# Performance work log

Hardware: AMD Instinct MI355X
Metric: run time of the kernel (lower is better)

## Reference

```python
import jax, jax.numpy as jnp
import numpy as np
from jax import lax

B, IN_N, OUT_N, SEQ, HID = 8, 16, 16, 256, 64
NUM_C = 64 + 3  # grid_size + spline_order
EPS_LN = 1e-5


def setup_inputs():
    key = jax.random.key(0)
    k = jax.random.split(key, 8)
    f32 = jnp.float32
    return {
        "x_in": jax.random.normal(k[0], (B, IN_N, SEQ, HID), f32),
        "proj_x_prev": jax.random.normal(k[1], (B, IN_N, SEQ, HID), f32),
        "spline_weights": jax.random.normal(k[2], (IN_N, OUT_N, NUM_C), f32) * 0.1,
        "base_scales": 0.6 + 0.1 * jax.random.normal(k[3], (IN_N, OUT_N), f32),
        "tau": jax.random.normal(k[4], (IN_N, OUT_N), f32) * 0.1 + 0.1,
        "temperature": jnp.array(1.0, f32),
        "omiga": jnp.full((IN_N, OUT_N), 0.2, f32),
        "W2": jax.random.normal(k[5], (OUT_N, HID, HID), f32) / np.sqrt(HID).astype(np.float32),
        "b_param": jnp.zeros((OUT_N, SEQ, HID), f32),
        "ln_w": jnp.ones((OUT_N, HID), f32),
        "ln_b": jnp.zeros((OUT_N, HID), f32),
        "alpha": jnp.full((OUT_N,), 0.5, f32),
        "beta": jnp.ones((OUT_N,), f32),
        "gamma": jnp.full((OUT_N,), 0.5, f32),
        "theta": jnp.ones((OUT_N,), f32),
        "conv_w": jax.random.normal(k[6], (OUT_N, HID, 1, 3, 3), f32) * 0.1,
    }


def _layernorm(x, w=None, b=None):
    mu = jnp.mean(x, -1, keepdims=True)
    var = jnp.mean((x - mu) ** 2, -1, keepdims=True)
    y = (x - mu) / jnp.sqrt(var + EPS_LN)
    if w is not None:
        y = y * w + b
    return y


def _dwconv(x, w):
    # x: [b, C, 16, 16]; w: [C, 1, 3, 3]; depthwise conv, SAME padding
    return lax.conv_general_dilated(
        x, w, (1, 1), "SAME",
        dimension_numbers=("NCHW", "OIHW", "NCHW"),
        feature_group_count=x.shape[1])


def _forward(x_in, proj_x_prev, spline_weights, base_scales, tau, temperature,
             omiga, W2, b_param, ln_w, ln_b, alpha, beta, gamma, theta, conv_w):
    b, in_n, seq, feat = x_in.shape
    num_c = spline_weights.shape[-1]
    grid = jnp.linspace(-1.0, 1.0, num_c)
    h = 2.0 / (num_c - 1)

    x_energy = jnp.mean(x_in, -1)  # [b,i,s]
    x_norm = jnp.clip(
        x_energy / (jnp.max(jnp.abs(x_energy), -1, keepdims=True) + 1e-8),
        -0.99, 0.99)

    # cubic B-spline basis (masked branches -> nested where)
    dist = jnp.abs(x_norm[..., None] - grid) / h  # [b,i,s,c]
    basis = jnp.where(dist < 1.0, 2.0 / 3.0 - dist ** 2 + dist ** 3 / 2.0,
            jnp.where(dist < 2.0, (2.0 - dist) ** 3 / 6.0, jnp.zeros_like(dist)))

    base_feat = jax.nn.silu(x_norm)[:, :, None, :] * base_scales[None, :, :, None]  # [b,i,j,s]
    spline_feat = jnp.einsum("bisc,ijc->bijs", basis, spline_weights)
    edge_resp = base_feat + spline_feat
    # [b,i,j,s,f]
    activated = (edge_resp[..., None] + jnp.abs(omiga)[None, :, :, None, None]) * x_in[:, :, None]

    t_val = jnp.abs(temperature) + 1e-4
    edge_energies = jnp.mean(jnp.abs(activated), axis=(-1, -2))  # [b,i,j]
    tau_abs = jnp.abs(tau)  # [i,j]
    mask = jax.nn.sigmoid((edge_energies - tau_abs[None]) / t_val)  # [b,i,j]

    # attention kernel W1, vectorized over output neuron j
    mid = in_n // 2
    mult = edge_energies / (tau_abs[None] + 1e-8)  # [b,i,j]
    wp = proj_x_prev[:, :, None] * (mult * mask)[..., None, None]  # [b,i,j,s,d]
    d = wp.shape[-1]
    K = jnp.transpose(wp[:, :mid], (0, 2, 3, 1, 4)).reshape(b, -1, seq, mid * d)
    Q = jnp.transpose(wp[:, mid:2 * mid], (0, 2, 3, 1, 4)).reshape(b, -1, seq, mid * d)
    K, Q = _layernorm(K), _layernorm(Q)
    raw = jnp.einsum("bjsk,bjtk->bjst", K, Q) / (jnp.sqrt(jnp.float32(mid * d)) * t_val)
    W1 = jax.nn.softmax(raw, axis=-1)  # [b,j,s,s]

    # masked mean over input neurons -> per-neuron SplineWeightLayer (vectorized)
    x = jnp.mean(activated * mask[..., None, None], axis=1)  # [b,j,s,f]
    xn = _layernorm(x, ln_w[None, :, None, :], ln_b[None, :, None, :])
    x_prime = jnp.einsum("bjsf,jfo->bjso", xn, W2) + b_param[None]  # [b,j,s,o]
    o = x_prime.shape[-1]

    # depthwise 3x3 conv on 16x16 spatial view, per-j kernels
    xsp = jnp.transpose(x_prime, (1, 0, 3, 2)).reshape(-1, b, o, 16, 16)  # [j,b,o,16,16]
    w3 = jax.vmap(_dwconv)(xsp, conv_w)  # [j,b,o,16,16]
    w3 = jnp.transpose(w3.reshape(-1, b, o, seq), (1, 0, 3, 2))  # [b,j,s,o]

    eye = jnp.eye(seq, dtype=x_prime.dtype)
    ak = (jnp.abs(beta)[None, :, None, None] * W1
          + jnp.abs(alpha)[None, :, None, None] * eye[None, None])
    glob = jnp.einsum("bjst,bjto->bjso", ak, x_prime)
    combined = glob + jnp.abs(theta)[None, :, None, None] * w3
    # residual_proj is Identity since in_hidden == out_hidden
    out = combined + gamma[None, :, None, None] * x
    return out, x_prime  # both [b, out_n, seq, out_hidden]


def reference(x_in, proj_x_prev, spline_weights, base_scales, tau, temperature,
              omiga, W2, b_param, ln_w, ln_b, alpha, beta, gamma, theta, conv_w):
    return _forward(x_in, proj_x_prev, spline_weights, base_scales, tau, temperature,
                    omiga, W2, b_param, ln_w, ln_b, alpha, beta, gamma, theta, conv_w)
```

## Files before the change

kernel.cpp:

```cpp
#include <hip/hip_runtime.h>

#define EPSLN 1e-5f

typedef short bf16x8 __attribute__((ext_vector_type(8)));
typedef float f32x4 __attribute__((ext_vector_type(4)));
typedef unsigned short u16;
typedef unsigned short u16x8 __attribute__((ext_vector_type(8)));

__device__ __forceinline__ float wsum(float v){
  #pragma unroll
  for(int o=32;o;o>>=1) v += __shfl_xor(v,o);
  return v;
}
__device__ __forceinline__ float wmax(float v){
  #pragma unroll
  for(int o=32;o;o>>=1) v = fmaxf(v,__shfl_xor(v,o));
  return v;
}
__device__ __forceinline__ u16 f2bf(float f){
  unsigned int u = __float_as_uint(f);
  u = (u + 0x7FFFu + ((u>>16)&1u)) >> 16;
  return (u16)u;
}
__device__ __forceinline__ float bf2f(u16 h){
  return __uint_as_float(((unsigned int)h)<<16);
}

__global__ void __launch_bounds__(256) kA(
                   const float* __restrict__ xin, const float* __restrict__ p,
                   const float* __restrict__ W2,
                   float* __restrict__ xe, float* __restrict__ xa,
                   float* __restrict__ Sv, float* __restrict__ SSv,
                   u16* __restrict__ xinb, u16* __restrict__ phi, u16* __restrict__ plo,
                   u16* __restrict__ w2B){
  int t = threadIdx.x;
  int rl = t>>3, q = t&7;
  int row = blockIdx.x*32 + rl;
  const float4* xr = (const float4*)(xin + row*64 + q*8);
  const float4* pr = (const float4*)(p   + row*64 + q*8);
  float s1=0.f,s2=0.f,s3=0.f,s4=0.f;
  u16x8 xb, ph, pl;
  #pragma unroll
  for(int k=0;k<2;k++){
    float4 xv = xr[k];
    float4 pv = pr[k];
    s1 += xv.x+xv.y+xv.z+xv.w;
    s2 += fabsf(xv.x)+fabsf(xv.y)+fabsf(xv.z)+fabsf(xv.w);
    s3 += pv.x+pv.y+pv.z+pv.w;
    s4 += pv.x*pv.x+pv.y*pv.y+pv.z*pv.z+pv.w*pv.w;
    int o = k*4;
    xb[o+0]=f2bf(xv.x); xb[o+1]=f2bf(xv.y); xb[o+2]=f2bf(xv.z); xb[o+3]=f2bf(xv.w);
    u16 h0=f2bf(pv.x), h1=f2bf(pv.y), h2=f2bf(pv.z), h3=f2bf(pv.w);
    ph[o+0]=h0; ph[o+1]=h1; ph[o+2]=h2; ph[o+3]=h3;
    pl[o+0]=f2bf(pv.x-bf2f(h0)); pl[o+1]=f2bf(pv.y-bf2f(h1));
    pl[o+2]=f2bf(pv.z-bf2f(h2)); pl[o+3]=f2bf(pv.w-bf2f(h3));
  }
  *(u16x8*)(xinb + row*64 + q*8) = xb;
  *(u16x8*)(phi  + row*64 + q*8) = ph;
  *(u16x8*)(plo  + row*64 + q*8) = pl;
  s1 += __shfl_xor(s1,1); s1 += __shfl_xor(s1,2); s1 += __shfl_xor(s1,4);
  s2 += __shfl_xor(s2,1); s2 += __shfl_xor(s2,2); s2 += __shfl_xor(s2,4);
  s3 += __shfl_xor(s3,1); s3 += __shfl_xor(s3,2); s3 += __shfl_xor(s3,4);
  s4 += __shfl_xor(s4,1); s4 += __shfl_xor(s4,2); s4 += __shfl_xor(s4,4);
  if(q==0){ xe[row]=s1*(1.f/64.f); xa[row]=s2*(1.f/64.f); Sv[row]=s3; SSv[row]=s4; }
  if(blockIdx.x<16){
    int j = blockIdx.x;
    for(int idx=threadIdx.x; idx<4096; idx+=256){
      int f = idx>>6, o = idx&63;
      float v = W2[j*4096 + idx];
      int ks = f>>5, kb = (f>>3)&3, i = f&7;
      int nt = o>>4, col = o&15;
      int ln = kb*16 + col;
      w2B[((j*2+ks)*4 + nt)*512 + ln*8 + i] = f2bf(v);
    }
  }
}

__global__ void __launch_bounds__(256) kBE(
                   const float* __restrict__ xe, const float* __restrict__ sw,
                   const float* __restrict__ bs, const float* __restrict__ om,
                   const float* __restrict__ xa, const float* __restrict__ tau,
                   const float* __restrict__ temp,
                   u16* __restrict__ er2b, float* __restrict__ mask,
                   float* __restrict__ cc,
                   const u16* __restrict__ phi, const u16* __restrict__ plo,
                   float* __restrict__ G){
  __shared__ __align__(16) unsigned char shm[32768];
  int tid = threadIdx.x;
  if(blockIdx.x < 128){
    float* swL = (float*)shm;
    float* bsL = swL + 1072;
    float* omL = bsL + 16;
    float* red = omL + 16;
    float* redE= red + 4;
    int bi = blockIdx.x;
    int i = bi & 15;
    int w = tid>>6, lane = tid&63;
    for(int k=tid;k<16*67;k+=256) swL[k] = sw[i*16*67 + k];
    if(tid<16){ bsL[tid]=bs[i*16+tid]; omL[tid]=fabsf(om[i*16+tid]); }
    float v = xe[bi*256+tid];
    float m = wmax(fabsf(v));
    if(lane==0) red[w]=m;
    __syncthreads();
    m = fmaxf(fmaxf(red[0],red[1]),fmaxf(red[2],red[3]));
    float xn = v/(m+1e-8f);
    xn = fminf(fmaxf(xn,-0.99f),0.99f);
    float sil = xn/(1.f+expf(-xn));
    float vv = (xn+1.f)*33.f;
    int c0 = (int)floorf(vv)-1;
    float acc[16];
    #pragma unroll
    for(int j=0;j<16;j++) acc[j]=0.f;
    #pragma unroll
    for(int k=0;k<4;k++){
      int c = c0+k;
      if(c<0||c>66) continue;
      float d = fabsf(vv-(float)c);
      float bas = d<1.f ? (2.f/3.f - d*d + d*d*d*0.5f)
                : (d<2.f ? (2.f-d)*(2.f-d)*(2.f-d)*(1.f/6.f) : 0.f);
      #pragma unroll
      for(int j=0;j<16;j++) acc[j] += bas*swL[j*67+c];
    }
    float xav = xa[bi*256+tid];
    u16 evb[16];
    #pragma unroll
    for(int j=0;j<16;j++){
      float ev = sil*bsL[j] + acc[j] + omL[j];
      evb[j] = f2bf(ev);
      float pe = wsum(fabsf(ev)*xav);
      if(lane==0) redE[j*4+w]=pe;
    }
    *(u16x8*)(er2b + ((size_t)bi*256+tid)*16    ) = *(u16x8*)&evb[0];
    *(u16x8*)(er2b + ((size_t)bi*256+tid)*16 + 8) = *(u16x8*)&evb[8];
    __syncthreads();
    if(tid<16){
      float e = (redE[tid*4+0]+redE[tid*4+1]+redE[tid*4+2]+redE[tid*4+3])*(1.f/256.f);
      float tv = fabsf(temp[0])+1e-4f;
      float ta = fabsf(tau[i*16+tid]);
      float mk = 1.f/(1.f+expf(-(e-ta)/tv));
      mask[bi*16+tid]=mk;
      cc[bi*16+tid]= e/(ta+1e-8f)*mk;
    }
  } else {
    u16* AfB = (u16*)shm;
    u16* BfB = AfB + 8192;
    int e = blockIdx.x - 128;
    int b = e&7, m = (e>>3)&7, sx = (e>>6)&3, ty = e>>8;
    int bm = b*8+m;
    int s0 = sx*64, t0 = ty*64;
    int row = tid>>2, dseg = tid&3;
    size_t offA = ((size_t)(b*16+m  )*256 + s0 + row)*64 + dseg*16;
    size_t offB = ((size_t)(b*16+m+8)*256 + t0 + row)*64 + dseg*16;
    int d0 = dseg*16;
    int ks0 = d0>>5, kb0 = (d0>>3)&3;
    int ks1 = (d0+8)>>5, kb1 = ((d0+8)>>3)&3;
    int lr = row&15, stile = row>>4;
    #define AOFF(h,stl,ks,ln) (((((h)*4+(stl))*2+(ks))*64 + (ln))*8)
    {
      uint4 v0 = *(const uint4*)(phi + offA);
      uint4 v1 = *(const uint4*)(phi + offA + 8);
      *(uint4*)(AfB + AOFF(0,stile,ks0,kb0*16+lr)) = v0;
      *(uint4*)(AfB + AOFF(0,stile,ks1,kb1*16+lr)) = v1;
      uint4 w0 = *(const uint4*)(plo + offA);
      uint4 w1 = *(const uint4*)(plo + offA + 8);
      *(uint4*)(AfB + AOFF(1,stile,ks0,kb0*16+lr)) = w0;
      *(uint4*)(AfB + AOFF(1,stile,ks1,kb1*16+lr)) = w1;
      uint4 x0 = *(const uint4*)(phi + offB);
      uint4 x1 = *(const uint4*)(phi + offB + 8);
      *(uint4*)(BfB + AOFF(0,stile,ks0,kb0*16+lr)) = x0;
      *(uint4*)(BfB + AOFF(0,stile,ks1,kb1*16+lr)) = x1;
      uint4 y0 = *(const uint4*)(plo + offB);
      uint4 y1 = *(const uint4*)(plo + offB + 8);
      *(uint4*)(BfB + AOFF(1,stile,ks0,kb0*16+lr)) = y0;
      *(uint4*)(BfB + AOFF(1,stile,ks1,kb1*16+lr)) = y1;
    }
    __syncthreads();
    int w = tid>>6, lane = tid&63;
    bf16x8 ah0 = *(const bf16x8*)(AfB + AOFF(0,w,0,lane));
    bf16x8 ah1 = *(const bf16x8*)(AfB + AOFF(0,w,1,lane));
    bf16x8 al0 = *(const bf16x8*)(AfB + AOFF(1,w,0,lane));
    bf16x8 al1 = *(const bf16x8*)(AfB + AOFF(1,w,1,lane));
    f32x4 acc[4];
    #pragma unroll
    for(int tt=0;tt<4;tt++) acc[tt] = (f32x4){0.f,0.f,0.f,0.f};
    #pragma unroll
    for(int tt=0;tt<4;tt++){
      bf16x8 bh0 = *(const bf16x8*)(BfB + AOFF(0,tt,0,lane));
      bf16x8 bh1 = *(const bf16x8*)(BfB + AOFF(0,tt,1,lane));
      bf16x8 bl0 = *(const bf16x8*)(BfB + AOFF(1,tt,0,lane));
      bf16x8 bl1 = *(const bf16x8*)(BfB + AOFF(1,tt,1,lane));
      acc[tt] = __builtin_amdgcn_mfma_f32_16x16x32_bf16(ah0, bh0, acc[tt], 0,0,0);
      acc[tt] = __builtin_amdgcn_mfma_f32_16x16x32_bf16(ah1, bh1, acc[tt], 0,0,0);
      acc[tt] = __builtin_amdgcn_mfma_f32_16x16x32_bf16(ah0, bl0, acc[tt], 0,0,0);
      acc[tt] = __builtin_amdgcn_mfma_f32_16x16x32_bf16(ah1, bl1, acc[tt], 0,0,0);
      acc[tt] = __builtin_amdgcn_mfma_f32_16x16x32_bf16(al0, bh0, acc[tt], 0,0,0);
      acc[tt] = __builtin_amdgcn_mfma_f32_16x16x32_bf16(al1, bh1, acc[tt], 0,0,0);
    }
    int col = lane&15, r4 = lane>>4;
    #pragma unroll
    for(int tt=0;tt<4;tt++){
      #pragma unroll
      for(int r=0;r<4;r++){
        G[((size_t)bm*256 + s0 + w*16 + r4*4 + r)*256 + t0 + tt*16 + col] = acc[tt][r];
      }
    }
    #undef AOFF
  }
}

__global__ void __launch_bounds__(256) kD(
                   const u16* __restrict__ xinb, const u16* __restrict__ er2b,
                   const float* __restrict__ mask, const u16* __restrict__ w2B,
                   const float* __restrict__ lnw, const float* __restrict__ lnb,
                   const float* __restrict__ bp,
                   u16* __restrict__ xoutb, float* __restrict__ xp,
                   u16* __restrict__ xpB,
                   const float* __restrict__ Sv, const float* __restrict__ SSv,
                   const float* __restrict__ cc,
                   float* __restrict__ mKv, float* __restrict__ rKv,
                   float* __restrict__ mQv, float* __restrict__ rQv){
  int bid = blockIdx.x;
  int tid = threadIdx.x;
  if(bid >= 1024){
    int sid = bid - 1024;
    int b = sid&7, j = sid>>3;
    int t = tid;
    float sk=0,ssk=0,sq=0,ssq=0;
    #pragma unroll
    for(int m=0;m<8;m++){
      float ck = cc[(b*16+m)*16+j];
      float cq = cc[(b*16+m+8)*16+j];
      sk  += ck*Sv[(b*16+m)*256+t];
      ssk += ck*ck*SSv[(b*16+m)*256+t];
      sq  += cq*Sv[(b*16+m+8)*256+t];
      ssq += cq*cq*SSv[(b*16+m+8)*256+t];
    }
    float mk = sk*(1.f/512.f);
    float vk = ssk*(1.f/512.f) - mk*mk;
    float mq = sq*(1.f/512.f);
    float vq = ssq*(1.f/512.f) - mq*mq;
    int o = (b*16+j)*256+t;
    mKv[o]=mk; rKv[o]=rsqrtf(vk+EPSLN);
    mQv[o]=mq; rQv[o]=rsqrtf(vq+EPSLN);
    return;
  }
  int b = bid&7, jq = (bid>>3)&7, st = bid>>6;
  int j0 = jq*2;
  int w = tid>>6, lane = tid&63;
  __shared__ __align__(16) u16 xnS[2][16*64];
  __shared__ float mcL[32];
  if(tid<32) mcL[tid] = mask[(b*16+(tid>>1))*16 + j0 + (tid&1)];
  __syncthreads();
  int ss = lane>>4, fq = lane&15;
  int sl = w*4 + ss;
  int s  = st*16 + sl;
  float a00=0.f,a01=0.f,a02=0.f,a03=0.f;
  float a10=0.f,a11=0.f,a12=0.f,a13=0.f;
  #pragma unroll
  for(int i=0;i<16;i++){
    unsigned int epk = *(const unsigned int*)(er2b + ((size_t)((b*16+i)*256+s))*16 + j0);
    float e0 = bf2f((u16)(epk&0xFFFFu))*mcL[i*2+0];
    float e1 = bf2f((u16)(epk>>16))   *mcL[i*2+1];
    ushort4 xv = *(const ushort4*)(xinb + ((size_t)(b*16+i)*256+s)*64 + fq*4);
    float x0=bf2f(xv.x), x1=bf2f(xv.y), x2=bf2f(xv.z), x3=bf2f(xv.w);
    a00 += e0*x0; a01 += e0*x1; a02 += e0*x2; a03 += e0*x3;
    a10 += e1*x0; a11 += e1*x1; a12 += e1*x2; a13 += e1*x3;
  }
  #pragma unroll
  for(int jj=0;jj<2;jj++){
    int j = j0+jj;
    int bj = b*16+j;
    float acc0 = (jj? a10:a00)*(1.f/16.f);
    float acc1 = (jj? a11:a01)*(1.f/16.f);
    float acc2 = (jj? a12:a02)*(1.f/16.f);
    float acc3 = (jj? a13:a03)*(1.f/16.f);
    {
      u16 pk[4]={f2bf(acc0),f2bf(acc1),f2bf(acc2),f2bf(acc3)};
      *(ushort4*)(xoutb + ((size_t)bj*256+s)*64 + fq*4) = *(ushort4*)pk;
    }
    float part = acc0+acc1+acc2+acc3;
    part += __shfl_xor(part,1); part += __shfl_xor(part,2);
    part += __shfl_xor(part,4); part += __shfl_xor(part,8);
    float mu = part*(1.f/64.f);
    float d0=acc0-mu, d1=acc1-mu, d2=acc2-mu, d3=acc3-mu;
    float p2 = d0*d0+d1*d1+d2*d2+d3*d3;
    p2 += __shfl_xor(p2,1); p2 += __shfl_xor(p2,2);
    p2 += __shfl_xor(p2,4); p2 += __shfl_xor(p2,8);
    float rstd = rsqrtf(p2*(1.f/64.f)+EPSLN);
    float4 lw4 = *(const float4*)(lnw + j*64 + fq*4);
    float4 lb4 = *(const float4*)(lnb + j*64 + fq*4);
    u16 xn[4] = { f2bf(d0*rstd*lw4.x + lb4.x), f2bf(d1*rstd*lw4.y + lb4.y),
                  f2bf(d2*rstd*lw4.z + lb4.z), f2bf(d3*rstd*lw4.w + lb4.w) };
    *(ushort4*)((unsigned char*)&xnS[jj][0] + ((sl*128 + fq*8) ^ ((sl&7)<<4))) = *(ushort4*)xn;
  }
  __syncthreads();
  int m = lane&15, kb = lane>>4;
  #pragma unroll
  for(int jj=0;jj<2;jj++){
    int j = j0+jj;
    int bj = b*16+j;
    f32x4 acc = {0.f,0.f,0.f,0.f};
    unsigned char* xnB = (unsigned char*)&xnS[jj][0];
    #pragma unroll
    for(int ks=0;ks<2;ks++){
      bf16x8 a = *(const bf16x8*)(xnB + ((m*128 + ks*64 + kb*16) ^ ((m&7)<<4)));
      bf16x8 bfr = *(const bf16x8*)(w2B + ((j*2+ks)*4 + w)*512 + lane*8);
      acc = __builtin_amdgcn_mfma_f32_16x16x32_bf16(a, bfr, acc, 0, 0, 0);
    }
    int f = w*16 + m;
    u16 pk[4];
    #pragma unroll
    for(int r=0;r<4;r++){
      int si = kb*4 + r;
      int s2 = st*16 + si;
      float xpr = acc[r] + bp[((size_t)j*256+s2)*64+f];
      xp[((size_t)bj*256+s2)*64+f] = xpr;
      pk[r] = f2bf(xpr);
    }
    int s0 = st*16 + kb*4;
    int flat = ((s0>>5)*4 + w)*512 + ((s0>>3)&3)*128 + m*8 + (s0&7);
    *(ushort4*)(xpB + (size_t)bj*16384 + flat) = *(ushort4*)pk;
  }
}

__global__ void __launch_bounds__(256) kF(
    const float* __restrict__ G, const float* __restrict__ cc,
    const float* __restrict__ mKv, const float* __restrict__ rKv,
    const float* __restrict__ mQv, const float* __restrict__ rQv,
    const float* __restrict__ xp, const u16* __restrict__ xpB,
    const float* __restrict__ cw,
    const u16* __restrict__ xarrb, const float* __restrict__ temp,
    const float* __restrict__ alpha, const float* __restrict__ beta,
    const float* __restrict__ gamma_, const float* __restrict__ theta,
    float* __restrict__ out){
  int b = blockIdx.x, jp = blockIdx.y, st = blockIdx.z;
  int j0 = jp*4;
  int tid = threadIdx.x, w = tid>>6, lane = tid&63;
  __shared__ __align__(16) unsigned char ovl[26112];
  unsigned char* prA = ovl;
  unsigned char* prB = ovl + 8192;
  float* xpT = (float*)ovl;
  float tv = fabsf(temp[0])+1e-4f;
  float inv = 1.f/(sqrtf(512.f)*tv);
  float aM0[8],aM1[8],aM2[8],aM3[8];
  #pragma unroll
  for(int m=0;m<8;m++){
    float4 ck = *(const float4*)(cc + (b*16+m  )*16 + j0);
    float4 cq = *(const float4*)(cc + (b*16+m+8)*16 + j0);
    aM0[m]=ck.x*cq.x; aM1[m]=ck.y*cq.y; aM2[m]=ck.z*cq.z; aM3[m]=ck.w*cq.w;
  }
  int bj0 = b*16+j0;
  float4 mQ4a = *(const float4*)(mQv + (size_t)(bj0  )*256 + lane*4);
  float4 rQ4a = *(const float4*)(rQv + (size_t)(bj0  )*256 + lane*4);
  float4 mQ4b = *(const float4*)(mQv + (size_t)(bj0+1)*256 + lane*4);
  float4 rQ4b = *(const float4*)(rQv + (size_t)(bj0+1)*256 + lane*4);
  float4 mQ4c = *(const float4*)(mQv + (size_t)(bj0+2)*256 + lane*4);
  float4 rQ4c = *(const float4*)(rQv + (size_t)(bj0+2)*256 + lane*4);
  float4 mQ4d = *(const float4*)(mQv + (size_t)(bj0+3)*256 + lane*4);
  float4 rQ4d = *(const float4*)(rQv + (size_t)(bj0+3)*256 + lane*4);
  const float* Gb = G + (size_t)(b*8)*65536;
  ushort4 pk2[4], pk3[4];
  #pragma unroll
  for(int q=0;q<4;q++){
    int si = w*4+q;
    int s = st*16 + si;
    f32x4 dt0={0.f,0.f,0.f,0.f}, dt1={0.f,0.f,0.f,0.f};
    f32x4 dt2={0.f,0.f,0.f,0.f}, dt3={0.f,0.f,0.f,0.f};
    #pragma unroll
    for(int m=0;m<8;m++){
      f32x4 g4 = *(const f32x4*)(Gb + (size_t)m*65536 + s*256 + lane*4);
      dt0 += aM0[m]*g4; dt1 += aM1[m]*g4;
      dt2 += aM2[m]*g4; dt3 += aM3[m]*g4;
    }
    #define SMK(JJ, DT, MQ, RQ, PKOUT) { \
      float mKs = 512.f*mKv[(size_t)(bj0+JJ)*256 + s], rKs = rKv[(size_t)(bj0+JJ)*256 + s]; \
      float e0 = __expf((DT[0] - mKs*MQ.x)*rKs*RQ.x*inv); \
      float e1 = __expf((DT[1] - mKs*MQ.y)*rKs*RQ.y*inv); \
      float e2 = __expf((DT[2] - mKs*MQ.z)*rKs*RQ.z*inv); \
      float e3 = __expf((DT[3] - mKs*MQ.w)*rKs*RQ.w*inv); \
      float isf = 1.f/wsum(e0+e1+e2+e3); \
      u16 pk[4] = {f2bf(e0*isf), f2bf(e1*isf), f2bf(e2*isf), f2bf(e3*isf)}; \
      PKOUT = *(ushort4*)pk; }
    ushort4 t0v, t1v;
    SMK(0, dt0, mQ4a, rQ4a, t0v)
    SMK(1, dt1, mQ4b, rQ4b, t1v)
    int poff = (si*512 + lane*8) ^ ((si&7)<<4);
    *(ushort4*)(prA + poff) = t0v;
    *(ushort4*)(prB + poff) = t1v;
    SMK(2, dt2, mQ4c, rQ4c, pk2[q])
    SMK(3, dt3, mQ4d, rQ4d, pk3[q])
    #undef SMK
  }
  __syncthreads();
  int m_ = lane&15, kb = lane>>4;
  f32x4 av0={0.f,0.f,0.f,0.f}, av1={0.f,0.f,0.f,0.f};
  f32x4 av2={0.f,0.f,0.f,0.f}, av3={0.f,0.f,0.f,0.f};
  const u16* xpB0 = xpB + (size_t)(bj0  )*16384;
  const u16* xpB1 = xpB + (size_t)(bj0+1)*16384;
  const u16* xpB2 = xpB + (size_t)(bj0+2)*16384;
  const u16* xpB3 = xpB + (size_t)(bj0+3)*16384;
  #pragma unroll
  for(int ks=0;ks<8;ks++){
    int aoff = (m_*512 + ks*64 + kb*16) ^ ((m_&7)<<4);
    int boff = ((ks*4 + w)*64 + lane)*8;
    bf16x8 a0 = *(const bf16x8*)(prA + aoff);
    bf16x8 a1 = *(const bf16x8*)(prB + aoff);
    av0 = __builtin_amdgcn_mfma_f32_16x16x32_bf16(a0, *(const bf16x8*)(xpB0 + boff), av0, 0,0,0);
    av1 = __builtin_amdgcn_mfma_f32_16x16x32_bf16(a1, *(const bf16x8*)(xpB1 + boff), av1, 0,0,0);
  }
  __syncthreads();
  #pragma unroll
  for(int q=0;q<4;q++){
    int si = w*4+q;
    int poff = (si*512 + lane*8) ^ ((si&7)<<4);
    *(ushort4*)(prA + poff) = pk2[q];
    *(ushort4*)(prB + poff) = pk3[q];
  }
  __syncthreads();
  #pragma unroll
  for(int ks=0;ks<8;ks++){
    int aoff = (m_*512 + ks*64 + kb*16) ^ ((m_&7)<<4);
    int boff = ((ks*4 + w)*64 + lane)*8;
    bf16x8 a2 = *(const bf16x8*)(prA + aoff);
    bf16x8 a3 = *(const bf16x8*)(prB + aoff);
    av2 = __builtin_amdgcn_mfma_f32_16x16x32_bf16(a2, *(const bf16x8*)(xpB2 + boff), av2, 0,0,0);
    av3 = __builtin_amdgcn_mfma_f32_16x16x32_bf16(a3, *(const bf16x8*)(xpB3 + boff), av3, 0,0,0);
  }
  int f = w*16 + m_;
  #pragma unroll
  for(int pass=0; pass<2; pass++){
    __syncthreads();
    for(int idx4 = tid; idx4 < 1536; idx4 += 256){
      int jj = idx4 / 768;
      int rem = idx4 - jj*768;
      int rr_i = rem >> 8;
      int pos = rem & 255;
      int ci = pos>>4, f4 = pos&15;
      int grow = st - 1 + rr_i;
      float4 v = {0.f,0.f,0.f,0.f};
      if(grow>=0 && grow<16){
        v = *(const float4*)(xp + ((size_t)(b*16+j0+pass*2+jj)*256 + grow*16 + ci)*64 + f4*4);
      }
      *(float4*)(xpT + ((jj*3+rr_i)*16+ci)*68 + f4*4) = v;
    }
    __syncthreads();
    #pragma unroll
    for(int jj=0;jj<2;jj++){
      int j = j0 + pass*2 + jj;
      int bj = b*16+j;
      f32x4 acc = pass==0 ? (jj?av1:av0) : (jj?av3:av2);
      float al = fabsf(alpha[j]), be=fabsf(beta[j]), th=fabsf(theta[j]), ga=gamma_[j];
      const float* wq = cw + (j*64+f)*9;
      float w0=wq[0],w1=wq[1],w2=wq[2],w3v=wq[3],w4=wq[4],w5=wq[5],w6=wq[6],w7=wq[7],w8=wq[8];
      #pragma unroll
      for(int r=0;r<4;r++){
        int si = kb*4 + r;
        int s = st*16 + si;
        float gl = acc[r];
        float cv=0.f;
        #pragma unroll
        for(int dr=0;dr<3;dr++){
          float kw0 = dr==0?w0:(dr==1?w3v:w6);
          float kw1 = dr==0?w1:(dr==1?w4:w7);
          float kw2 = dr==0?w2:(dr==1?w5:w8);
          const float* rowp = xpT + ((jj*3+dr)*16)*68;
          if(si>0)  cv += rowp[(si-1)*68+f]*kw0;
                    cv += rowp[(si  )*68+f]*kw1;
          if(si<15) cv += rowp[(si+1)*68+f]*kw2;
        }
        float diag = xpT[((jj*3+1)*16+si)*68+f];
        size_t gi = ((size_t)bj*256+s)*64+f;
        out[gi] = be*gl + al*diag + th*cv + ga*bf2f(xarrb[gi]);
      }
    }
  }
}

extern "C" void kernel_launch(void* const* d_in, const int* in_sizes, int n_in,
                              void* d_out, int out_size, void* d_ws, size_t ws_size,
                              hipStream_t stream) {
  const float* xin = (const float*)d_in[0];
  const float* pxp = (const float*)d_in[1];
  const float* sw  = (const float*)d_in[2];
  const float* bs  = (const float*)d_in[3];
  const float* tau = (const float*)d_in[4];
  const float* temp= (const float*)d_in[5];
  const float* om  = (const float*)d_in[6];
  const float* W2  = (const float*)d_in[7];
  const float* bp  = (const float*)d_in[8];
  const float* lnw = (const float*)d_in[9];
  const float* lnb = (const float*)d_in[10];
  const float* alpha=(const float*)d_in[11];
  const float* beta= (const float*)d_in[12];
  const float* gam = (const float*)d_in[13];
  const float* theta=(const float*)d_in[14];
  const float* cw  = (const float*)d_in[15];
  float* outp = (float*)d_out;
  float* xpo  = outp + 2097152;

  float* ws  = (float*)d_ws;
  float* xe  = ws;
  float* xa  = xe + 32768;
  float* Sv  = xa + 32768;
  float* SSv = Sv + 32768;
  u16*   er2b= (u16*)(SSv + 32768);
  float* mask= (float*)(er2b) + 524288;
  float* ccv = mask + 2048;
  float* mKv = ccv + 2048;
  float* rKv = mKv + 32768;
  float* mQv = rKv + 32768;
  float* rQv = mQv + 32768;
  float* Gv  = rQv + 32768;
  u16* xvb = (u16*)(Gv + 4194304);
  u16* xpB = xvb + 2097152;
  u16* w2B = xpB + 2097152;
  u16* xinb= w2B + 65536;
  u16* phi = xinb + 2097152;
  u16* plo = phi + 2097152;

  kA<<<1024,256,0,stream>>>(xin,pxp,W2,xe,xa,Sv,SSv,xinb,phi,plo,w2B);
  kBE<<<1152,256,0,stream>>>(xe,sw,bs,om,xa,tau,temp,er2b,mask,ccv,phi,plo,Gv);
  kD<<<1152,256,0,stream>>>(xinb,er2b,mask,w2B,lnw,lnb,bp,xvb,xpo,xpB,
                            Sv,SSv,ccv,mKv,rKv,mQv,rQv);
  kF<<<dim3(8,4,16),256,0,stream>>>(Gv,ccv,mKv,rKv,mQv,rQv,xpo,xpB,cw,xvb,temp,
                                    alpha,beta,gam,theta,outp);
}
```

Measured before the change: 52.66 us.

## Regroup four kernels into three by merging independent stages per launch

The old kA, kBE and kD kernels become k1 and k2. The spline/energy blocks now compute the row mean and absolute mean of x_in directly from global memory, instead of waiting for a separate pre-pass, so they can share a launch with the bf16 conversion blocks. The Gram-matrix MFMA blocks now share a launch with the mixing/LayerNorm/W2 blocks and the stats blocks, since those stages do not depend on each other. This removes one launch and the xe/xa intermediates, at the cost of each spline thread reading a full 64-float row on its own (uncoalesced strided access) and k2 mixing block types with different shared-memory and register needs.

New measurement: 50.32 us (median of 2 runs). 1.05x faster.

```diff
diff --git a/kernel.cpp b/kernel.cpp
--- a/kernel.cpp
+++ b/kernel.cpp
@@ -26,69 +26,19 @@
   return __uint_as_float(((unsigned int)h)<<16);
 }
 
-__global__ void __launch_bounds__(256) kA(
-                   const float* __restrict__ xin, const float* __restrict__ p,
-                   const float* __restrict__ W2,
-                   float* __restrict__ xe, float* __restrict__ xa,
-                   float* __restrict__ Sv, float* __restrict__ SSv,
-                   u16* __restrict__ xinb, u16* __restrict__ phi, u16* __restrict__ plo,
-                   u16* __restrict__ w2B){
-  int t = threadIdx.x;
-  int rl = t>>3, q = t&7;
-  int row = blockIdx.x*32 + rl;
-  const float4* xr = (const float4*)(xin + row*64 + q*8);
-  const float4* pr = (const float4*)(p   + row*64 + q*8);
-  float s1=0.f,s2=0.f,s3=0.f,s4=0.f;
-  u16x8 xb, ph, pl;
-  #pragma unroll
-  for(int k=0;k<2;k++){
-    float4 xv = xr[k];
-    float4 pv = pr[k];
-    s1 += xv.x+xv.y+xv.z+xv.w;
-    s2 += fabsf(xv.x)+fabsf(xv.y)+fabsf(xv.z)+fabsf(xv.w);
-    s3 += pv.x+pv.y+pv.z+pv.w;
-    s4 += pv.x*pv.x+pv.y*pv.y+pv.z*pv.z+pv.w*pv.w;
-    int o = k*4;
-    xb[o+0]=f2bf(xv.x); xb[o+1]=f2bf(xv.y); xb[o+2]=f2bf(xv.z); xb[o+3]=f2bf(xv.w);
-    u16 h0=f2bf(pv.x), h1=f2bf(pv.y), h2=f2bf(pv.z), h3=f2bf(pv.w);
-    ph[o+0]=h0; ph[o+1]=h1; ph[o+2]=h2; ph[o+3]=h3;
-    pl[o+0]=f2bf(pv.x-bf2f(h0)); pl[o+1]=f2bf(pv.y-bf2f(h1));
-    pl[o+2]=f2bf(pv.z-bf2f(h2)); pl[o+3]=f2bf(pv.w-bf2f(h3));
-  }
-  *(u16x8*)(xinb + row*64 + q*8) = xb;
-  *(u16x8*)(phi  + row*64 + q*8) = ph;
-  *(u16x8*)(plo  + row*64 + q*8) = pl;
-  s1 += __shfl_xor(s1,1); s1 += __shfl_xor(s1,2); s1 += __shfl_xor(s1,4);
-  s2 += __shfl_xor(s2,1); s2 += __shfl_xor(s2,2); s2 += __shfl_xor(s2,4);
-  s3 += __shfl_xor(s3,1); s3 += __shfl_xor(s3,2); s3 += __shfl_xor(s3,4);
-  s4 += __shfl_xor(s4,1); s4 += __shfl_xor(s4,2); s4 += __shfl_xor(s4,4);
-  if(q==0){ xe[row]=s1*(1.f/64.f); xa[row]=s2*(1.f/64.f); Sv[row]=s3; SSv[row]=s4; }
-  if(blockIdx.x<16){
-    int j = blockIdx.x;
-    for(int idx=threadIdx.x; idx<4096; idx+=256){
-      int f = idx>>6, o = idx&63;
-      float v = W2[j*4096 + idx];
-      int ks = f>>5, kb = (f>>3)&3, i = f&7;
-      int nt = o>>4, col = o&15;
-      int ln = kb*16 + col;
-      w2B[((j*2+ks)*4 + nt)*512 + ln*8 + i] = f2bf(v);
-    }
-  }
-}
-
-__global__ void __launch_bounds__(256) kBE(
-                   const float* __restrict__ xe, const float* __restrict__ sw,
-                   const float* __restrict__ bs, const float* __restrict__ om,
-                   const float* __restrict__ xa, const float* __restrict__ tau,
-                   const float* __restrict__ temp,
-                   u16* __restrict__ er2b, float* __restrict__ mask,
-                   float* __restrict__ cc,
-                   const u16* __restrict__ phi, const u16* __restrict__ plo,
-                   float* __restrict__ G){
-  __shared__ __align__(16) unsigned char shm[32768];
+__global__ void __launch_bounds__(256) k1(
+    const float* __restrict__ xin, const float* __restrict__ pxp,
+    const float* __restrict__ W2,  const float* __restrict__ sw,
+    const float* __restrict__ bs,  const float* __restrict__ om,
+    const float* __restrict__ tau, const float* __restrict__ temp,
+    float* __restrict__ Sv, float* __restrict__ SSv,
+    u16* __restrict__ xinb, u16* __restrict__ phi, u16* __restrict__ plo,
+    u16* __restrict__ w2B,
+    u16* __restrict__ er2b, float* __restrict__ mask, float* __restrict__ cc){
+  __shared__ float shmF[1172];
   int tid = threadIdx.x;
   if(blockIdx.x < 128){
-    float* swL = (float*)shm;
+    float* swL = shmF;
     float* bsL = swL + 1072;
     float* omL = bsL + 16;
     float* red = omL + 16;
@@ -98,7 +48,18 @@
     int w = tid>>6, lane = tid&63;
     for(int k=tid;k<16*67;k+=256) swL[k] = sw[i*16*67 + k];
     if(tid<16){ bsL[tid]=bs[i*16+tid]; omL[tid]=fabsf(om[i*16+tid]); }
-    float v = xe[bi*256+tid];
+    float xs=0.f, xas=0.f;
+    {
+      const float4* xr = (const float4*)(xin + ((size_t)bi*256 + tid)*64);
+      #pragma unroll
+      for(int k=0;k<16;k++){
+        float4 v4 = xr[k];
+        xs  += v4.x+v4.y+v4.z+v4.w;
+        xas += fabsf(v4.x)+fabsf(v4.y)+fabsf(v4.z)+fabsf(v4.w);
+      }
+    }
+    float v   = xs *(1.f/64.f);
+    float xav = xas*(1.f/64.f);
     float m = wmax(fabsf(v));
     if(lane==0) red[w]=m;
     __syncthreads();
@@ -121,7 +82,6 @@
       #pragma unroll
       for(int j=0;j<16;j++) acc[j] += bas*swL[j*67+c];
     }
-    float xav = xa[bi*256+tid];
     u16 evb[16];
     #pragma unroll
     for(int j=0;j<16;j++){
@@ -142,9 +102,64 @@
       cc[bi*16+tid]= e/(ta+1e-8f)*mk;
     }
   } else {
+    int ab = blockIdx.x - 128;
+    int rl = tid>>3, q = tid&7;
+    int row = ab*32 + rl;
+    const float4* xr = (const float4*)(xin + row*64 + q*8);
+    const float4* pr = (const float4*)(pxp + row*64 + q*8);
+    float s3=0.f,s4=0.f;
+    u16x8 xb, ph, pl;
+    #pragma unroll
+    for(int k=0;k<2;k++){
+      float4 xv = xr[k];
+      float4 pv = pr[k];
+      s3 += pv.x+pv.y+pv.z+pv.w;
+      s4 += pv.x*pv.x+pv.y*pv.y+pv.z*pv.z+pv.w*pv.w;
+      int o = k*4;
+      xb[o+0]=f2bf(xv.x); xb[o+1]=f2bf(xv.y); xb[o+2]=f2bf(xv.z); xb[o+3]=f2bf(xv.w);
+      u16 h0=f2bf(pv.x), h1=f2bf(pv.y), h2=f2bf(pv.z), h3=f2bf(pv.w);
+      ph[o+0]=h0; ph[o+1]=h1; ph[o+2]=h2; ph[o+3]=h3;
+      pl[o+0]=f2bf(pv.x-bf2f(h0)); pl[o+1]=f2bf(pv.y-bf2f(h1));
+      pl[o+2]=f2bf(pv.z-bf2f(h2)); pl[o+3]=f2bf(pv.w-bf2f(h3));
+    }
+    *(u16x8*)(xinb + row*64 + q*8) = xb;
+    *(u16x8*)(phi  + row*64 + q*8) = ph;
+    *(u16x8*)(plo  + row*64 + q*8) = pl;
+    s3 += __shfl_xor(s3,1); s3 += __shfl_xor(s3,2); s3 += __shfl_xor(s3,4);
+    s4 += __shfl_xor(s4,1); s4 += __shfl_xor(s4,2); s4 += __shfl_xor(s4,4);
+    if(q==0){ Sv[row]=s3; SSv[row]=s4; }
+    if(ab<16){
+      int j = ab;
+      for(int idx=tid; idx<4096; idx+=256){
+        int f = idx>>6, o = idx&63;
+        float vw = W2[j*4096 + idx];
+        int ks = f>>5, kb = (f>>3)&3, ii = f&7;
+        int nt = o>>4, col = o&15;
+        int ln = kb*16 + col;
+        w2B[((j*2+ks)*4 + nt)*512 + ln*8 + ii] = f2bf(vw);
+      }
+    }
+  }
+}
+
+__global__ void __launch_bounds__(256) k2(
+    const u16* __restrict__ phi, const u16* __restrict__ plo, float* __restrict__ G,
+    const u16* __restrict__ xinb, const u16* __restrict__ er2b,
+    const float* __restrict__ mask, const u16* __restrict__ w2B,
+    const float* __restrict__ lnw, const float* __restrict__ lnb,
+    const float* __restrict__ bp,
+    u16* __restrict__ xvb, float* __restrict__ xp, u16* __restrict__ xpB,
+    const float* __restrict__ Sv, const float* __restrict__ SSv,
+    const float* __restrict__ cc,
+    float* __restrict__ mKv, float* __restrict__ rKv,
+    float* __restrict__ mQv, float* __restrict__ rQv){
+  __shared__ __align__(16) unsigned char shm[32768];
+  int tid = threadIdx.x;
+  int bid = blockIdx.x;
+  if(bid < 1024){
     u16* AfB = (u16*)shm;
     u16* BfB = AfB + 8192;
-    int e = blockIdx.x - 128;
+    int e = bid;
     int b = e&7, m = (e>>3)&7, sx = (e>>6)&3, ty = e>>8;
     int bm = b*8+m;
     int s0 = sx*64, t0 = ty*64;
@@ -205,24 +220,87 @@
       }
     }
     #undef AOFF
-  }
-}
-
-__global__ void __launch_bounds__(256) kD(
-                   const u16* __restrict__ xinb, const u16* __restrict__ er2b,
-                   const float* __restrict__ mask, const u16* __restrict__ w2B,
-                   const float* __restrict__ lnw, const float* __restrict__ lnb,
-                   const float* __restrict__ bp,
-                   u16* __restrict__ xoutb, float* __restrict__ xp,
-                   u16* __restrict__ xpB,
-                   const float* __restrict__ Sv, const float* __restrict__ SSv,
-                   const float* __restrict__ cc,
-                   float* __restrict__ mKv, float* __restrict__ rKv,
-                   float* __restrict__ mQv, float* __restrict__ rQv){
-  int bid = blockIdx.x;
-  int tid = threadIdx.x;
-  if(bid >= 1024){
-    int sid = bid - 1024;
+  } else if(bid < 2048){
+    int idx = bid - 1024;
+    int b = idx&7, jq = (idx>>3)&7, st = idx>>6;
+    int j0 = jq*2;
+    int w = tid>>6, lane = tid&63;
+    u16* xnS = (u16*)shm;
+    float* mcL = (float*)(shm + 4096);
+    if(tid<32) mcL[tid] = mask[(b*16+(tid>>1))*16 + j0 + (tid&1)];
+    __syncthreads();
+    int ss = lane>>4, fq = lane&15;
+    int sl = w*4 + ss;
+    int s  = st*16 + sl;
+    float a00=0.f,a01=0.f,a02=0.f,a03=0.f;
+    float a10=0.f,a11=0.f,a12=0.f,a13=0.f;
+    #pragma unroll
+    for(int i=0;i<16;i++){
+      unsigned int epk = *(const unsigned int*)(er2b + ((size_t)((b*16+i)*256+s))*16 + j0);
+      float e0 = bf2f((u16)(epk&0xFFFFu))*mcL[i*2+0];
+      float e1 = bf2f((u16)(epk>>16))   *mcL[i*2+1];
+      ushort4 xv = *(const ushort4*)(xinb + ((size_t)(b*16+i)*256+s)*64 + fq*4);
+      float x0=bf2f(xv.x), x1=bf2f(xv.y), x2=bf2f(xv.z), x3=bf2f(xv.w);
+      a00 += e0*x0; a01 += e0*x1; a02 += e0*x2; a03 += e0*x3;
+      a10 += e1*x0; a11 += e1*x1; a12 += e1*x2; a13 += e1*x3;
+    }
+    #pragma unroll
+    for(int jj=0;jj<2;jj++){
+      int j = j0+jj;
+      int bj = b*16+j;
+      float acc0 = (jj? a10:a00)*(1.f/16.f);
+      float acc1 = (jj? a11:a01)*(1.f/16.f);
+      float acc2 = (jj? a12:a02)*(1.f/16.f);
+      float acc3 = (jj? a13:a03)*(1.f/16.f);
+      {
+        u16 pk[4]={f2bf(acc0),f2bf(acc1),f2bf(acc2),f2bf(acc3)};
+        *(ushort4*)(xvb + ((size_t)bj*256+s)*64 + fq*4) = *(ushort4*)pk;
+      }
+      float part = acc0+acc1+acc2+acc3;
+      part += __shfl_xor(part,1); part += __shfl_xor(part,2);
+      part += __shfl_xor(part,4); part += __shfl_xor(part,8);
+      float mu = part*(1.f/64.f);
+      float d0=acc0-mu, d1=acc1-mu, d2=acc2-mu, d3=acc3-mu;
+      float p2 = d0*d0+d1*d1+d2*d2+d3*d3;
+      p2 += __shfl_xor(p2,1); p2 += __shfl_xor(p2,2);
+      p2 += __shfl_xor(p2,4); p2 += __shfl_xor(p2,8);
+      float rstd = rsqrtf(p2*(1.f/64.f)+EPSLN);
+      float4 lw4 = *(const float4*)(lnw + j*64 + fq*4);
+      float4 lb4 = *(const float4*)(lnb + j*64 + fq*4);
+      u16 xn[4] = { f2bf(d0*rstd*lw4.x + lb4.x), f2bf(d1*rstd*lw4.y + lb4.y),
+                    f2bf(d2*rstd*lw4.z + lb4.z), f2bf(d3*rstd*lw4.w + lb4.w) };
+      *(ushort4*)((unsigned char*)(xnS + jj*1024) + ((sl*128 + fq*8) ^ ((sl&7)<<4))) = *(ushort4*)xn;
+    }
+    __syncthreads();
+    int m = lane&15, kb = lane>>4;
+    #pragma unroll
+    for(int jj=0;jj<2;jj++){
+      int j = j0+jj;
+      int bj = b*16+j;
+      f32x4 acc = {0.f,0.f,0.f,0.f};
+      unsigned char* xnB = (unsigned char*)(xnS + jj*1024);
+      #pragma unroll
+      for(int ks=0;ks<2;ks++){
+        bf16x8 a = *(const bf16x8*)(xnB + ((m*128 + ks*64 + kb*16) ^ ((m&7)<<4)));
+        bf16x8 bfr = *(const bf16x8*)(w2B + ((j*2+ks)*4 + w)*512 + lane*8);
+        acc = __builtin_amdgcn_mfma_f32_16x16x32_bf16(a, bfr, acc, 0, 0, 0);
+      }
+      int f = w*16 + m;
+      u16 pk[4];
+      #pragma unroll
+      for(int r=0;r<4;r++){
+        int si = kb*4 + r;
+        int s2 = st*16 + si;
+        float xpr = acc[r] + bp[((size_t)j*256+s2)*64+f];
+        xp[((size_t)bj*256+s2)*64+f] = xpr;
+        pk[r] = f2bf(xpr);
+      }
+      int s0 = st*16 + kb*4;
+      int flat = ((s0>>5)*4 + w)*512 + ((s0>>3)&3)*128 + m*8 + (s0&7);
+      *(ushort4*)(xpB + (size_t)bj*16384 + flat) = *(ushort4*)pk;
+    }
+  } else {
+    int sid = bid - 2048;
     int b = sid&7, j = sid>>3;
     int t = tid;
     float sk=0,ssk=0,sq=0,ssq=0;
@@ -242,84 +320,6 @@
     int o = (b*16+j)*256+t;
     mKv[o]=mk; rKv[o]=rsqrtf(vk+EPSLN);
     mQv[o]=mq; rQv[o]=rsqrtf(vq+EPSLN);
-    return;
-  }
-  int b = bid&7, jq = (bid>>3)&7, st = bid>>6;
-  int j0 = jq*2;
-  int w = tid>>6, lane = tid&63;
-  __shared__ __align__(16) u16 xnS[2][16*64];
-  __shared__ float mcL[32];
-  if(tid<32) mcL[tid] = mask[(b*16+(tid>>1))*16 + j0 + (tid&1)];
-  __syncthreads();
-  int ss = lane>>4, fq = lane&15;
-  int sl = w*4 + ss;
-  int s  = st*16 + sl;
-  float a00=0.f,a01=0.f,a02=0.f,a03=0.f;
-  float a10=0.f,a11=0.f,a12=0.f,a13=0.f;
-  #pragma unroll
-  for(int i=0;i<16;i++){
-    unsigned int epk = *(const unsigned int*)(er2b + ((size_t)((b*16+i)*256+s))*16 + j0);
-    float e0 = bf2f((u16)(epk&0xFFFFu))*mcL[i*2+0];
-    float e1 = bf2f((u16)(epk>>16))   *mcL[i*2+1];
-    ushort4 xv = *(const ushort4*)(xinb + ((size_t)(b*16+i)*256+s)*64 + fq*4);
-    float x0=bf2f(xv.x), x1=bf2f(xv.y), x2=bf2f(xv.z), x3=bf2f(xv.w);
-    a00 += e0*x0; a01 += e0*x1; a02 += e0*x2; a03 += e0*x3;
-    a10 += e1*x0; a11 += e1*x1; a12 += e1*x2; a13 += e1*x3;
-  }
-  #pragma unroll
-  for(int jj=0;jj<2;jj++){
-    int j = j0+jj;
-    int bj = b*16+j;
-    float acc0 = (jj? a10:a00)*(1.f/16.f);
-    float acc1 = (jj? a11:a01)*(1.f/16.f);
-    float acc2 = (jj? a12:a02)*(1.f/16.f);
-    float acc3 = (jj? a13:a03)*(1.f/16.f);
-    {
-      u16 pk[4]={f2bf(acc0),f2bf(acc1),f2bf(acc2),f2bf(acc3)};
-      *(ushort4*)(xoutb + ((size_t)bj*256+s)*64 + fq*4) = *(ushort4*)pk;
-    }
-    float part = acc0+acc1+acc2+acc3;
-    part += __shfl_xor(part,1); part += __shfl_xor(part,2);
-    part += __shfl_xor(part,4); part += __shfl_xor(part,8);
-    float mu = part*(1.f/64.f);
-    float d0=acc0-mu, d1=acc1-mu, d2=acc2-mu, d3=acc3-mu;
-    float p2 = d0*d0+d1*d1+d2*d2+d3*d3;
-    p2 += __shfl_xor(p2,1); p2 += __shfl_xor(p2,2);
-    p2 += __shfl_xor(p2,4); p2 += __shfl_xor(p2,8);
-    float rstd = rsqrtf(p2*(1.f/64.f)+EPSLN);
-    float4 lw4 = *(const float4*)(lnw + j*64 + fq*4);
-    float4 lb4 = *(const float4*)(lnb + j*64 + fq*4);
-    u16 xn[4] = { f2bf(d0*rstd*lw4.x + lb4.x), f2bf(d1*rstd*lw4.y + lb4.y),
-                  f2bf(d2*rstd*lw4.z + lb4.z), f2bf(d3*rstd*lw4.w + lb4.w) };
-    *(ushort4*)((unsigned char*)&xnS[jj][0] + ((sl*128 + fq*8) ^ ((sl&7)<<4))) = *(ushort4*)xn;
-  }
-  __syncthreads();
-  int m = lane&15, kb = lane>>4;
-  #pragma unroll
-  for(int jj=0;jj<2;jj++){
-    int j = j0+jj;
-    int bj = b*16+j;
-    f32x4 acc = {0.f,0.f,0.f,0.f};
-    unsigned char* xnB = (unsigned char*)&xnS[jj][0];
-    #pragma unroll
-    for(int ks=0;ks<2;ks++){
-      bf16x8 a = *(const bf16x8*)(xnB + ((m*128 + ks*64 + kb*16) ^ ((m&7)<<4)));
-      bf16x8 bfr = *(const bf16x8*)(w2B + ((j*2+ks)*4 + w)*512 + lane*8);
-      acc = __builtin_amdgcn_mfma_f32_16x16x32_bf16(a, bfr, acc, 0, 0, 0);
-    }
-    int f = w*16 + m;
-    u16 pk[4];
-    #pragma unroll
-    for(int r=0;r<4;r++){
-      int si = kb*4 + r;
-      int s2 = st*16 + si;
-      float xpr = acc[r] + bp[((size_t)j*256+s2)*64+f];
-      xp[((size_t)bj*256+s2)*64+f] = xpr;
-      pk[r] = f2bf(xpr);
-    }
-    int s0 = st*16 + kb*4;
-    int flat = ((s0>>5)*4 + w)*512 + ((s0>>3)&3)*128 + m*8 + (s0&7);
-    *(ushort4*)(xpB + (size_t)bj*16384 + flat) = *(ushort4*)pk;
   }
 }
 
@@ -499,9 +499,7 @@
   float* xpo  = outp + 2097152;
 
   float* ws  = (float*)d_ws;
-  float* xe  = ws;
-  float* xa  = xe + 32768;
-  float* Sv  = xa + 32768;
+  float* Sv  = ws;
   float* SSv = Sv + 32768;
   u16*   er2b= (u16*)(SSv + 32768);
   float* mask= (float*)(er2b) + 524288;
@@ -518,10 +516,10 @@
   u16* phi = xinb + 2097152;
   u16* plo = phi + 2097152;
 
-  kA<<<1024,256,0,stream>>>(xin,pxp,W2,xe,xa,Sv,SSv,xinb,phi,plo,w2B);
-  kBE<<<1152,256,0,stream>>>(xe,sw,bs,om,xa,tau,temp,er2b,mask,ccv,phi,plo,Gv);
-  kD<<<1152,256,0,stream>>>(xinb,er2b,mask,w2B,lnw,lnb,bp,xvb,xpo,xpB,
-                            Sv,SSv,ccv,mKv,rKv,mQv,rQv);
+  k1<<<1152,256,0,stream>>>(xin,pxp,W2,sw,bs,om,tau,temp,
+                            Sv,SSv,xinb,phi,plo,w2B,er2b,mask,ccv);
+  k2<<<2176,256,0,stream>>>(phi,plo,Gv,xinb,er2b,mask,w2B,lnw,lnb,bp,
+                            xvb,xpo,xpB,Sv,SSv,ccv,mKv,rKv,mQv,rQv);
   kF<<<dim3(8,4,16),256,0,stream>>>(Gv,ccv,mKv,rKv,mQv,rQv,xpo,xpB,cw,xvb,temp,
                                     alpha,beta,gam,theta,outp);
 }
```
